# Kernel optimization log

Hardware: AMD Instinct MI355X
Metric: run time of the kernel (lower is better)

Reference implementation:

```python
import jax, jax.numpy as jnp
import numpy as np

ALPHA = 0.2  # LeakyReLU negative slope


def setup_inputs() -> dict:
    key = jax.random.key(0)
    ks = jax.random.split(key, 7)
    B, Wn, K, E, O = 16, 64, 256, 128, 64
    s = lambda k, shape, fan: jax.random.normal(k, shape, jnp.float32) * (1.0 / np.sqrt(fan))
    return {
        "x": jax.random.normal(ks[0], (B, Wn, K), jnp.float32),
        "lin_w": s(ks[1], (E, 2 * Wn), 2 * Wn),   # torch Linear weight (out,in)
        "lin_b": jnp.zeros((E,), jnp.float32),
        "a": s(ks[2], (E,), E),
        "bias_kk": s(ks[3], (K, K), K) * 0.1,
        "fc_w": s(ks[4], (O, K), K),
        "fc_b": jnp.zeros((O,), jnp.float32),
    }


def reference(x, lin_w, lin_b, a, bias_kk, fc_w, fc_b):
    # x: (B, W, K) -> v: (B, K, W); K nodes, W features per node
    v = jnp.transpose(x, (0, 2, 1))
    Wn = v.shape[-1]
    # lin(concat(v_i, v_j)) == v_i @ W1^T + v_j @ W2^T + b  (avoids O(K^2*2W) concat)
    W1, W2 = lin_w[:, :Wn], lin_w[:, Wn:]
    left = jnp.einsum("bkw,ew->bke", v, W1)   # (B,K,E)
    right = jnp.einsum("bkw,ew->bke", v, W2)  # (B,K,E)
    g = left[:, :, None, :] + right[:, None, :, :] + lin_b  # (B,K,K,E)
    g = jnp.where(g >= 0, g, ALPHA * g)  # LeakyReLU
    e = jnp.einsum("bije,e->bij", g, a) + bias_kk  # (B,K,K)
    attn = jax.nn.softmax(e, axis=2)
    # dropout p=0.0 / eval mode -> identity
    h = jax.nn.sigmoid(jnp.einsum("bij,bjw->biw", attn, v))  # (B,K,W)
    out = jnp.einsum("bwk,ok->bwo", jnp.transpose(h, (0, 2, 1)), fc_w) + fc_b
    return out  # (B, W, out_dim)
```

## Files before the change

### kernel.cpp

```cpp
#include <hip/hip_runtime.h>
#include <hip/hip_bf16.h>

#define ALPHA 0.2f
#define C1 0.6f
#define C2 0.4f

__global__ __launch_bounds__(256) void k_proj(
    const float* __restrict__ x, const float* __restrict__ lin_w,
    float* __restrict__ left, float* __restrict__ right, float* __restrict__ v) {
  const int xcd = blockIdx.x & 7;
  const int s   = blockIdx.x >> 3;
  const int b   = 2 * xcd + (s & 1);
  const int k0  = (s >> 1) * 8;
  const int tid = threadIdx.x;

  __shared__ float s_x[8][68];

  {
    const int w  = tid >> 2;
    const int kq = tid & 3;
    float2 xv = *(const float2*)(x + b * 16384 + w * 256 + k0 + kq * 2);
    s_x[kq * 2 + 0][w] = xv.x;
    s_x[kq * 2 + 1][w] = xv.y;
  }
  __syncthreads();

  if (tid < 128) {
    const int k  = tid >> 4;
    const int wq = tid & 15;
    float4 vv = *(const float4*)&s_x[k][wq * 4];
    *(float4*)(v + (b * 256 + k0 + k) * 64 + wq * 4) = vv;
  }

  const int e  = tid & 127;
  const int kh = tid >> 7;
  float accL[4] = {0, 0, 0, 0};
  float accR[4] = {0, 0, 0, 0};
  const float4* w1 = (const float4*)(lin_w + e * 128);
  const float4* w2 = w1 + 16;
#pragma unroll
  for (int wc = 0; wc < 16; ++wc) {
    float4 l = w1[wc];
    float4 r = w2[wc];
#pragma unroll
    for (int k = 0; k < 4; ++k) {
      float4 sx = *(const float4*)&s_x[kh * 4 + k][wc * 4];
      accL[k] += sx.x * l.x + sx.y * l.y + sx.z * l.z + sx.w * l.w;
      accR[k] += sx.x * r.x + sx.y * r.y + sx.z * r.z + sx.w * r.w;
    }
  }
#pragma unroll
  for (int k = 0; k < 4; ++k) {
    int kk = (b * 256 + k0 + kh * 4 + k) * 128 + e;
    left[kk]  = accL[k];
    right[kk] = accR[k];
  }
}

__global__ __launch_bounds__(256) void k_attn(
    const float* __restrict__ left, const float* __restrict__ right,
    const float* __restrict__ lin_b, const float* __restrict__ a,
    const float* __restrict__ bias_kk, const float* __restrict__ v,
    float* __restrict__ h) {
  const int xcd = blockIdx.x & 7;
  const int sblk = blockIdx.x >> 3;
  const int b   = 2 * xcd + (sblk & 1);
  const int i0  = (sblk >> 1) * 8;
  const int tid = threadIdx.x;

  __shared__ float s_lb[8][132];
  __shared__ float s_a[128];
  __shared__ float s_ca[128];
  __shared__ float s_AL[8];
  __shared__ float s_sc[8][260];
  __shared__ float s_inv[8];
  __shared__ float s_v[128][68];

  float bk[8];
#pragma unroll
  for (int i = 0; i < 8; ++i) bk[i] = bias_kk[(i0 + i) * 256 + tid];

  if (tid < 128) {
    float av = a[tid];
    s_a[tid]  = av;
    s_ca[tid] = C2 * av;
  }
  {
    const int ii = tid >> 5;
    const int e4 = (tid & 31) * 4;
    float4 lv = *(const float4*)(left + (b * 256 + i0 + ii) * 128 + e4);
    float4 bv = *(const float4*)(lin_b + e4);
    lv.x += bv.x; lv.y += bv.y; lv.z += bv.z; lv.w += bv.w;
    *(float4*)&s_lb[ii][e4] = lv;
  }
  __syncthreads();

  {
    const int ii = tid >> 5, sl = tid & 31;
    float p = 0.f;
#pragma unroll
    for (int m = 0; m < 4; ++m) p += s_a[sl * 4 + m] * s_lb[ii][sl * 4 + m];
#pragma unroll
    for (int off = 16; off > 0; off >>= 1) p += __shfl_xor(p, off, 64);
    if (sl == 0) s_AL[ii] = p;
  }

  float acc[8];
#pragma unroll
  for (int i = 0; i < 8; ++i) acc[i] = 0.f;
  float ar = 0.f;
  const float4* rp = (const float4*)(right + (b * 256 + tid) * 128);
#pragma unroll
  for (int ec = 0; ec < 8; ++ec) {
    float4 r0 = rp[ec * 4 + 0], r1 = rp[ec * 4 + 1],
           r2 = rp[ec * 4 + 2], r3 = rp[ec * 4 + 3];
    float4 a0 = *(const float4*)&s_a[ec * 16 + 0];
    float4 a1 = *(const float4*)&s_a[ec * 16 + 4];
    float4 a2 = *(const float4*)&s_a[ec * 16 + 8];
    float4 a3 = *(const float4*)&s_a[ec * 16 + 12];
    ar += a0.x * r0.x + a0.y * r0.y + a0.z * r0.z + a0.w * r0.w;
    ar += a1.x * r1.x + a1.y * r1.y + a1.z * r1.z + a1.w * r1.w;
    ar += a2.x * r2.x + a2.y * r2.y + a2.z * r2.z + a2.w * r2.w;
    ar += a3.x * r3.x + a3.y * r3.y + a3.z * r3.z + a3.w * r3.w;
    float4 c0 = *(const float4*)&s_ca[ec * 16 + 0];
    float4 c1 = *(const float4*)&s_ca[ec * 16 + 4];
    float4 c2 = *(const float4*)&s_ca[ec * 16 + 8];
    float4 c3 = *(const float4*)&s_ca[ec * 16 + 12];
#pragma unroll
    for (int i = 0; i < 8; ++i) {
      float4 l0 = *(const float4*)&s_lb[i][ec * 16 + 0];
      float4 l1 = *(const float4*)&s_lb[i][ec * 16 + 4];
      float4 l2 = *(const float4*)&s_lb[i][ec * 16 + 8];
      float4 l3 = *(const float4*)&s_lb[i][ec * 16 + 12];
      float t, s = acc[i];
      t = l0.x + r0.x; s = fmaf(c0.x, fabsf(t), s);
      t = l0.y + r0.y; s = fmaf(c0.y, fabsf(t), s);
      t = l0.z + r0.z; s = fmaf(c0.z, fabsf(t), s);
      t = l0.w + r0.w; s = fmaf(c0.w, fabsf(t), s);
      t = l1.x + r1.x; s = fmaf(c1.x, fabsf(t), s);
      t = l1.y + r1.y; s = fmaf(c1.y, fabsf(t), s);
      t = l1.z + r1.z; s = fmaf(c1.z, fabsf(t), s);
      t = l1.w + r1.w; s = fmaf(c1.w, fabsf(t), s);
      t = l2.x + r2.x; s = fmaf(c2.x, fabsf(t), s);
      t = l2.y + r2.y; s = fmaf(c2.y, fabsf(t), s);
      t = l2.z + r2.z; s = fmaf(c2.z, fabsf(t), s);
      t = l2.w + r2.w; s = fmaf(c2.w, fabsf(t), s);
      t = l3.x + r3.x; s = fmaf(c3.x, fabsf(t), s);
      t = l3.y + r3.y; s = fmaf(c3.y, fabsf(t), s);
      t = l3.z + r3.z; s = fmaf(c3.z, fabsf(t), s);
      t = l3.w + r3.w; s = fmaf(c3.w, fabsf(t), s);
      acc[i] = s;
    }
  }
  __syncthreads();

#pragma unroll
  for (int i = 0; i < 8; ++i) {
    float sc = fmaf(C1, s_AL[i] + ar, acc[i]) + bk[i];
    s_sc[i][tid] = __expf(sc);
  }
  __syncthreads();

  {
    const int wv = tid >> 6, lane = tid & 63;
#pragma unroll
    for (int rr = 0; rr < 2; ++rr) {
      int i = wv * 2 + rr;
      float s = s_sc[i][lane] + s_sc[i][lane + 64] +
                s_sc[i][lane + 128] + s_sc[i][lane + 192];
#pragma unroll
      for (int off = 32; off > 0; off >>= 1) s += __shfl_xor(s, off, 64);
      if (lane == 0) s_inv[i] = 1.f / s;
    }
  }

  const int iq = tid >> 5;
  const int w  = (tid & 31) * 2;
  float h0 = 0.f, h1 = 0.f;
#pragma unroll
  for (int c = 0; c < 2; ++c) {
    __syncthreads();
#pragma unroll
    for (int t = 0; t < 8; ++t) {
      int idx = tid + t * 256;
      int row = idx >> 4, col = (idx & 15) * 4;
      *(float4*)&s_v[row][col] =
          *(const float4*)(v + (b * 256 + c * 128 + row) * 64 + col);
    }
    __syncthreads();
#pragma unroll 4
    for (int jj = 0; jj < 128; jj += 4) {
      float4 at = *(const float4*)&s_sc[iq][c * 128 + jj];
      float2 v0 = *(const float2*)&s_v[jj + 0][w];
      float2 v1 = *(const float2*)&s_v[jj + 1][w];
      float2 v2 = *(const float2*)&s_v[jj + 2][w];
      float2 v3 = *(const float2*)&s_v[jj + 3][w];
      h0 += at.x * v0.x + at.y * v1.x + at.z * v2.x + at.w * v3.x;
      h1 += at.x * v0.y + at.y * v1.y + at.z * v2.y + at.w * v3.y;
    }
  }
  float inv = s_inv[iq];
  float2 hv;
  hv.x = 1.f / (1.f + __expf(-h0 * inv));
  hv.y = 1.f / (1.f + __expf(-h1 * inv));
  *(float2*)(h + (b * 256 + i0 + iq) * 64 + w) = hv;
}

__global__ __launch_bounds__(256) void k_out(
    const float* __restrict__ h, const float* __restrict__ fc_w,
    const float* __restrict__ fc_b, float* __restrict__ out) {
  const int xcd = blockIdx.x & 7;
  const int s   = blockIdx.x >> 3;
  const int b   = 2 * xcd + (s & 1);
  const int wg  = s >> 1;
  const int wl  = threadIdx.x >> 6;
  const int o   = threadIdx.x & 63;
  const int w   = wg * 4 + wl;

  __shared__ float s_h[256 * 4];
  for (int idx = threadIdx.x; idx < 1024; idx += 256) {
    int k = idx >> 2, wl2 = idx & 3;
    s_h[idx] = h[(b * 256 + k) * 64 + wg * 4 + wl2];
  }
  __syncthreads();

  float acc = 0.f;
  const float4* fw = (const float4*)(fc_w + o * 256);
#pragma unroll
  for (int k4 = 0; k4 < 64; ++k4) {
    float4 f = fw[k4];
    int k = k4 * 4;
    acc += s_h[(k + 0) * 4 + wl] * f.x + s_h[(k + 1) * 4 + wl] * f.y +
           s_h[(k + 2) * 4 + wl] * f.z + s_h[(k + 3) * 4 + wl] * f.w;
  }
  out[b * 64 * 64 + w * 64 + o] = acc + fc_b[o];
}

extern "C" void kernel_launch(void* const* d_in, const int* in_sizes, int n_in,
                              void* d_out, int out_size, void* d_ws, size_t ws_size,
                              hipStream_t stream) {
  const float* x       = (const float*)d_in[0];
  const float* lin_w   = (const float*)d_in[1];
  const float* lin_b   = (const float*)d_in[2];
  const float* a       = (const float*)d_in[3];
  const float* bias_kk = (const float*)d_in[4];
  const float* fc_w    = (const float*)d_in[5];
  const float* fc_b    = (const float*)d_in[6];
  float* out = (float*)d_out;

  float* ws    = (float*)d_ws;
  float* left  = ws;
  float* right = ws + 524288;
  float* v     = ws + 1048576;
  float* h     = ws + 1310720;

  k_proj<<<512, 256, 0, stream>>>(x, lin_w, left, right, v);
  k_attn<<<512, 256, 0, stream>>>(left, right, lin_b, a, bias_kk, v, h);
  k_out<<<256, 256, 0, stream>>>(h, fc_w, fc_b, out);
}
```

Before: 104.3 us.

## Prefetch right rows to registers and stream V into LDS asynchronously

The attention kernel now loads each thread's full row of `right` into 32 float4 registers up front. It issues `global_load_lds` copies of the whole 256x64 V tile into shared memory early, so those copies overlap with the score computation. This removes the two-chunk V staging loop and its extra barriers, and keeps the softmax inverses in registers instead of shared memory. The costs are much higher register and LDS use (a 64KB V buffer), with `launch_bounds` requesting 2 blocks per CU, which could cause spills or lower occupancy. The waves read the `s_sc` rows that belong to them for the inverse, which relies on `iq` mapping to the wave's two rows.

New measurement: 108.4 us. 3.9% more time.

```diff
diff --git a/kernel.cpp b/kernel.cpp
--- a/kernel.cpp
+++ b/kernel.cpp
@@ -4,6 +4,13 @@
 #define ALPHA 0.2f
 #define C1 0.6f
 #define C2 0.4f
+
+typedef const __attribute__((address_space(1))) float gas_float;
+typedef __attribute__((address_space(3))) float las_float;
+
+__device__ __forceinline__ void gld_lds16(const float* g, float* l) {
+  __builtin_amdgcn_global_load_lds((gas_float*)g, (las_float*)l, 16, 0, 0);
+}
 
 __global__ __launch_bounds__(256) void k_proj(
     const float* __restrict__ x, const float* __restrict__ lin_w,
@@ -57,7 +64,7 @@
   }
 }
 
-__global__ __launch_bounds__(256) void k_attn(
+__global__ __launch_bounds__(256, 2) void k_attn(
     const float* __restrict__ left, const float* __restrict__ right,
     const float* __restrict__ lin_b, const float* __restrict__ a,
     const float* __restrict__ bias_kk, const float* __restrict__ v,
@@ -73,8 +80,7 @@
   __shared__ float s_ca[128];
   __shared__ float s_AL[8];
   __shared__ float s_sc[8][260];
-  __shared__ float s_inv[8];
-  __shared__ float s_v[128][68];
+  __shared__ float s_v[256][64];
 
   float bk[8];
 #pragma unroll
@@ -95,6 +101,22 @@
   }
   __syncthreads();
 
+  const float4* rp = (const float4*)(right + (b * 256 + tid) * 128);
+  float4 r[32];
+#pragma unroll
+  for (int q = 0; q < 32; ++q) r[q] = rp[q];
+
+  {
+    const int seg0 = (tid >> 6) * 16;
+    const int ln4  = (tid & 63) * 4;
+    const float* vb = v + b * 16384;
+#pragma unroll
+    for (int t = 0; t < 16; ++t) {
+      const int seg = seg0 + t;
+      gld_lds16(vb + seg * 256 + ln4, &s_v[0][0] + seg * 256);
+    }
+  }
+
   {
     const int ii = tid >> 5, sl = tid & 31;
     float p = 0.f;
@@ -109,11 +131,10 @@
 #pragma unroll
   for (int i = 0; i < 8; ++i) acc[i] = 0.f;
   float ar = 0.f;
-  const float4* rp = (const float4*)(right + (b * 256 + tid) * 128);
 #pragma unroll
   for (int ec = 0; ec < 8; ++ec) {
-    float4 r0 = rp[ec * 4 + 0], r1 = rp[ec * 4 + 1],
-           r2 = rp[ec * 4 + 2], r3 = rp[ec * 4 + 3];
+    float4 r0 = r[ec * 4 + 0], r1 = r[ec * 4 + 1],
+           r2 = r[ec * 4 + 2], r3 = r[ec * 4 + 3];
     float4 a0 = *(const float4*)&s_a[ec * 16 + 0];
     float4 a1 = *(const float4*)&s_a[ec * 16 + 4];
     float4 a2 = *(const float4*)&s_a[ec * 16 + 8];
@@ -161,45 +182,36 @@
   }
   __syncthreads();
 
+  float invA, invB;
   {
     const int wv = tid >> 6, lane = tid & 63;
-#pragma unroll
-    for (int rr = 0; rr < 2; ++rr) {
-      int i = wv * 2 + rr;
-      float s = s_sc[i][lane] + s_sc[i][lane + 64] +
-                s_sc[i][lane + 128] + s_sc[i][lane + 192];
-#pragma unroll
-      for (int off = 32; off > 0; off >>= 1) s += __shfl_xor(s, off, 64);
-      if (lane == 0) s_inv[i] = 1.f / s;
-    }
+    float sA = s_sc[2 * wv + 0][lane] + s_sc[2 * wv + 0][lane + 64] +
+               s_sc[2 * wv + 0][lane + 128] + s_sc[2 * wv + 0][lane + 192];
+    float sB = s_sc[2 * wv + 1][lane] + s_sc[2 * wv + 1][lane + 64] +
+               s_sc[2 * wv + 1][lane + 128] + s_sc[2 * wv + 1][lane + 192];
+#pragma unroll
+    for (int off = 32; off > 0; off >>= 1) {
+      sA += __shfl_xor(sA, off, 64);
+      sB += __shfl_xor(sB, off, 64);
+    }
+    invA = 1.f / sA;
+    invB = 1.f / sB;
   }
 
   const int iq = tid >> 5;
   const int w  = (tid & 31) * 2;
   float h0 = 0.f, h1 = 0.f;
-#pragma unroll
-  for (int c = 0; c < 2; ++c) {
-    __syncthreads();
-#pragma unroll
-    for (int t = 0; t < 8; ++t) {
-      int idx = tid + t * 256;
-      int row = idx >> 4, col = (idx & 15) * 4;
-      *(float4*)&s_v[row][col] =
-          *(const float4*)(v + (b * 256 + c * 128 + row) * 64 + col);
-    }
-    __syncthreads();
 #pragma unroll 4
-    for (int jj = 0; jj < 128; jj += 4) {
-      float4 at = *(const float4*)&s_sc[iq][c * 128 + jj];
-      float2 v0 = *(const float2*)&s_v[jj + 0][w];
-      float2 v1 = *(const float2*)&s_v[jj + 1][w];
-      float2 v2 = *(const float2*)&s_v[jj + 2][w];
-      float2 v3 = *(const float2*)&s_v[jj + 3][w];
-      h0 += at.x * v0.x + at.y * v1.x + at.z * v2.x + at.w * v3.x;
-      h1 += at.x * v0.y + at.y * v1.y + at.z * v2.y + at.w * v3.y;
-    }
-  }
-  float inv = s_inv[iq];
+  for (int jj = 0; jj < 256; jj += 4) {
+    float4 at = *(const float4*)&s_sc[iq][jj];
+    float2 v0 = *(const float2*)&s_v[jj + 0][w];
+    float2 v1 = *(const float2*)&s_v[jj + 1][w];
+    float2 v2 = *(const float2*)&s_v[jj + 2][w];
+    float2 v3 = *(const float2*)&s_v[jj + 3][w];
+    h0 += at.x * v0.x + at.y * v1.x + at.z * v2.x + at.w * v3.x;
+    h1 += at.x * v0.y + at.y * v1.y + at.z * v2.y + at.w * v3.y;
+  }
+  const float inv = (iq & 1) ? invB : invA;
   float2 hv;
   hv.x = 1.f / (1.f + __expf(-h0 * inv));
   hv.y = 1.f / (1.f + __expf(-h1 * inv));
```
